# Kernel optimization log

Hardware: AMD Instinct MI355X
Metric: run time of the kernel (lower is better)

Reference implementation:

```python
import jax, jax.numpy as jnp
import numpy as np

N_NODES = 100000
N_EDGES = 3200000
N_FEAT = 500
N_HID = 256
N_CLASS = 40


def spmm(edge_row, edge_col, edge_val, x, num_nodes):
    # out[i] = sum_{e: row[e]==i} val[e] * x[col[e]]
    msgs = edge_val[:, None] * x[edge_col]          # [E, F] gather + scale
    return jax.ops.segment_sum(msgs, edge_row, num_segments=num_nodes)


def setup_inputs() -> dict:
    key = jax.random.key(0)
    k1, k2, k3, k4, k5, k6, k7, k8 = jax.random.split(key, 8)
    features = jax.random.normal(k1, (N_NODES, N_FEAT), dtype=jnp.float32)
    edge_row = jax.random.randint(k2, (N_EDGES,), 0, N_NODES, dtype=jnp.int32)
    edge_col = jax.random.randint(k3, (N_EDGES,), 0, N_NODES, dtype=jnp.int32)
    edge_val = jax.random.uniform(k4, (N_EDGES,), dtype=jnp.float32)
    # Xavier-uniform linear weights, zero biases (as in reset_parameters)
    lim1 = float(np.sqrt(6.0 / (N_FEAT + N_HID)))
    W1 = jax.random.uniform(k5, (N_FEAT, N_HID), minval=-lim1, maxval=lim1, dtype=jnp.float32)
    b1 = jnp.zeros((N_HID,), dtype=jnp.float32)
    lim2 = float(np.sqrt(6.0 / (N_HID + N_CLASS)))
    W2 = jax.random.uniform(k6, (N_HID, N_CLASS), minval=-lim2, maxval=lim2, dtype=jnp.float32)
    b2 = jnp.zeros((N_CLASS,), dtype=jnp.float32)
    return {
        "features": features,
        "edge_row": edge_row,
        "edge_col": edge_col,
        "edge_val": edge_val,
        "W1": W1, "b1": b1, "W2": W2, "b2": b2,
    }


def reference(features, edge_row, edge_col, edge_val, W1, b1, W2, b2):
    # Layer 1: linear -> spmm -> relu   (eval mode: dropout is identity)
    h = features @ W1 + b1                          # [N, nhid]
    h = spmm(edge_row, edge_col, edge_val, h, N_NODES)
    h = jax.nn.relu(h)
    # Layer 2: linear -> spmm
    o = h @ W2 + b2                                 # [N, nclass]
    o = spmm(edge_row, edge_col, edge_val, o, N_NODES)
    return jax.nn.log_softmax(o, axis=1)
```

## Files before the change

kernel.cpp:

```cpp
#include <hip/hip_runtime.h>
#include <hip/hip_bf16.h>
#include <math.h>

#define N_NODES 100000
#define N_FEAT 500
#define N_HID 256
#define N_CLASS 40

typedef float f32x4 __attribute__((ext_vector_type(4)));
typedef float f32x2 __attribute__((ext_vector_type(2)));
typedef int i32x4 __attribute__((ext_vector_type(4)));
typedef unsigned int u32x4 __attribute__((ext_vector_type(4)));
typedef short short8 __attribute__((ext_vector_type(8)));
typedef unsigned short u16x8 __attribute__((ext_vector_type(8)));

__device__ __forceinline__ float b2f(unsigned short u) {
  union { unsigned int i; float f; } c; c.i = ((unsigned int)u) << 16; return c.f;
}
__device__ __forceinline__ unsigned short f2bu(float x) {
  __hip_bfloat16 b = __float2bfloat16(x);
  union { __hip_bfloat16 b; unsigned short u; } c; c.b = b; return c.u;
}
__device__ __forceinline__ float decode_val(unsigned int p) {
  union { unsigned int i; float f; } c; c.i = (p & 0x7FFFu) << 17; return c.f;
}
__device__ __forceinline__ unsigned char f2fp8(float x) {
  return (unsigned char)(__builtin_amdgcn_cvt_pk_fp8_f32(x, x, 0, false) & 0xFF);
}
__device__ __forceinline__ void gload_lds16(const void* gptr, void* lptr) {
  __builtin_amdgcn_global_load_lds(
      (const __attribute__((address_space(1))) unsigned int*)gptr,
      (__attribute__((address_space(3))) unsigned int*)lptr, 16, 0, 0);
}

__global__ __launch_bounds__(256) void prep_kernel(
    const float* __restrict__ W1, unsigned short* __restrict__ Bsw,
    const int* __restrict__ er, const int* __restrict__ ec,
    const float* __restrict__ ev, int* __restrict__ cnt,
    unsigned int* __restrict__ cvps, int E) {
  if (blockIdx.x < 64) {
    int t = blockIdx.x * 256 + threadIdx.x;
    int col = t >> 6, ch = t & 63;
    int g = ch >> 3, c = ch & 7;
    int c_src = c ^ (col & 7);
    int k = g * 64 + c_src * 8;
    u16x8 o;
#pragma unroll
    for (int j = 0; j < 8; j++) {
      int kk = k + j;
      o[j] = (kk < N_FEAT) ? f2bu(W1[(size_t)kk * N_HID + col]) : (unsigned short)0;
    }
    *(u16x8*)(Bsw + (size_t)col * 512 + g * 64 + c * 8) = o;
  }
  int nv = E >> 2;
  int t = blockIdx.x * 256 + threadIdx.x;
  int nthr = gridDim.x * 256;
  const i32x4* er4 = (const i32x4*)er;
  const i32x4* ec4 = (const i32x4*)ec;
  const f32x4* ev4 = (const f32x4*)ev;
  for (int i = t; i < nv; i += nthr) {
    i32x4 r = __builtin_nontemporal_load(&er4[i]);
    i32x4 c = __builtin_nontemporal_load(&ec4[i]);
    f32x4 v = __builtin_nontemporal_load(&ev4[i]);
    atomicAdd(&cnt[r.x], 1);
    atomicAdd(&cnt[r.y], 1);
    atomicAdd(&cnt[r.z], 1);
    atomicAdd(&cnt[r.w], 1);
    u32x4 pk;
    pk.x = ((unsigned int)c.x << 15) | ((unsigned int)f2bu(v.x) >> 1);
    pk.y = ((unsigned int)c.y << 15) | ((unsigned int)f2bu(v.y) >> 1);
    pk.z = ((unsigned int)c.z << 15) | ((unsigned int)f2bu(v.z) >> 1);
    pk.w = ((unsigned int)c.w << 15) | ((unsigned int)f2bu(v.w) >> 1);
    __builtin_nontemporal_store(pk, (u32x4*)(cvps + 4 * (size_t)i));
  }
  int tail = nv << 2;
  if (blockIdx.x == 0 && threadIdx.x < E - tail) {
    int i = tail + threadIdx.x;
    atomicAdd(&cnt[er[i]], 1);
    cvps[i] = ((unsigned int)ec[i] << 15) | ((unsigned int)f2bu(ev[i]) >> 1);
  }
}

__global__ __launch_bounds__(1024) void scan1_kernel(
    int* __restrict__ cnt, int* __restrict__ bsum, int n) {
  __shared__ int wsum[16];
  int tid = threadIdx.x, lane = tid & 63, wid = tid >> 6;
  int i = blockIdx.x * 1024 + tid;
  int v = (i < n) ? cnt[i] : 0;
  int x = v;
#pragma unroll
  for (int off = 1; off < 64; off <<= 1) {
    int t = __shfl_up(x, off);
    if (lane >= off) x += t;
  }
  if (lane == 63) wsum[wid] = x;
  __syncthreads();
  if (tid < 16) {
    int ws = wsum[tid];
#pragma unroll
    for (int off = 1; off < 16; off <<= 1) {
      int t = __shfl_up(ws, off);
      if (tid >= off) ws += t;
    }
    wsum[tid] = ws;
  }
  __syncthreads();
  int excl = (wid ? wsum[wid - 1] : 0) + x - v;
  if (i < n) cnt[i] = excl;
  if (tid == 0) bsum[blockIdx.x] = wsum[15];
}

__global__ __launch_bounds__(64) void scan2_kernel(
    int* __restrict__ bsum, int* __restrict__ row_ptr, int nb, int n) {
  int lane = threadIdx.x;
  int carry = 0;
  for (int base = 0; base < nb; base += 64) {
    int i = base + lane;
    int v = (i < nb) ? bsum[i] : 0;
    int x = v;
#pragma unroll
    for (int off = 1; off < 64; off <<= 1) {
      int t = __shfl_up(x, off);
      if (lane >= off) x += t;
    }
    if (i < nb) bsum[i] = carry + x - v;
    carry += __shfl(x, 63);
  }
  if (lane == 0) row_ptr[n] = carry;
}

__global__ __launch_bounds__(256) void scan3_kernel(
    int* __restrict__ cnt, const int* __restrict__ bsum,
    int* __restrict__ row_ptr, int n) {
  int i = blockIdx.x * 256 + threadIdx.x;
  if (i >= n) return;
  int v = cnt[i] + bsum[i >> 10];
  cnt[i] = v;
  row_ptr[i] = v;
}

__global__ __launch_bounds__(256) void fused_sg(
    const int* __restrict__ er, const unsigned int* __restrict__ cvps,
    int* __restrict__ cursor, unsigned int* __restrict__ cvp, int E,
    const float* __restrict__ A, const unsigned short* __restrict__ Bsw,
    const float* __restrict__ b1, unsigned char* __restrict__ H, int M,
    int SB) {
  __shared__ __align__(16) char smem[36864];
  if ((int)blockIdx.x < SB) {
    int sb = blockIdx.x;
    int s = sb & 3;
    int g = sb >> 2;
    int ngrp = SB >> 2;
    int nv = E >> 2;
    const i32x4* er4 = (const i32x4*)er;
    const u32x4* cv4 = (const u32x4*)cvps;
    for (int i = g * 256 + threadIdx.x; i < nv; i += ngrp * 256) {
      i32x4 r = __builtin_nontemporal_load(&er4[i]);
      u32x4 p = __builtin_nontemporal_load(&cv4[i]);
      if (((r.x >> 9) & 3) == s) cvp[atomicAdd(&cursor[r.x], 1)] = p.x;
      if (((r.y >> 9) & 3) == s) cvp[atomicAdd(&cursor[r.y], 1)] = p.y;
      if (((r.z >> 9) & 3) == s) cvp[atomicAdd(&cursor[r.z], 1)] = p.z;
      if (((r.w >> 9) & 3) == s) cvp[atomicAdd(&cursor[r.w], 1)] = p.w;
    }
    int tail = nv << 2;
    if (sb == 0 && threadIdx.x < E - tail) {
      int i = tail + threadIdx.x;
      cvp[atomicAdd(&cursor[er[i]], 1)] = cvps[i];
    }
    return;
  }
  int gb = blockIdx.x - SB;
  char* sA = smem;
  char* sB = smem + 4096;
  int tid = threadIdx.x;
  int lane = tid & 63, w = tid >> 6;
  int wc = w;
  int bm = gb * 32;

  f32x4 acc[2][4];
#pragma unroll
  for (int m = 0; m < 2; m++)
#pragma unroll
    for (int n = 0; n < 4; n++) acc[m][n] = (f32x4)0.f;

  for (int s = 0; s < 8; s++) {
    int k0 = s * 64;
#pragma unroll
    for (int i = 0; i < 2; i++) {
      int f4 = i * 256 + tid;
      int row = f4 >> 4, cidx = f4 & 15;
      int grow = bm + row;
      int k = k0 + cidx * 4;
      float4 v = make_float4(0.f, 0.f, 0.f, 0.f);
      if (grow < M && k < N_FEAT) v = *(const float4*)(A + (size_t)grow * N_FEAT + k);
      ushort4 u;
      u.x = f2bu(v.x); u.y = f2bu(v.y); u.z = f2bu(v.z); u.w = f2bu(v.w);
      int chunk = cidx >> 1, sub = cidx & 1;
      int byte = row * 128 + (((chunk ^ (row & 7))) << 4) + (sub << 3);
      *(ushort4*)(sA + byte) = u;
    }
#pragma unroll
    for (int j = 0; j < 8; j++) {
      int base = j * 4096 + w * 1024;
      int L = base + lane * 16;
      int col = L >> 7, c = (L >> 4) & 7;
      const char* gp = (const char*)Bsw + (size_t)col * 1024 + s * 128 + c * 16;
      gload_lds16(gp, sB + base);
    }
    __syncthreads();
#pragma unroll
    for (int kk = 0; kk < 2; kk++) {
      int cw = kk * 4 + (lane >> 4);
      short8 af[2], bg[4];
#pragma unroll
      for (int m = 0; m < 2; m++) {
        int ar = m * 16 + (lane & 15);
        af[m] = *(const short8*)(sA + ar * 128 + ((cw ^ (ar & 7)) << 4));
      }
#pragma unroll
      for (int n = 0; n < 4; n++) {
        int bc = wc * 64 + n * 16 + (lane & 15);
        bg[n] = *(const short8*)(sB + bc * 128 + ((cw ^ (bc & 7)) << 4));
      }
#pragma unroll
      for (int m = 0; m < 2; m++)
#pragma unroll
        for (int n = 0; n < 4; n++)
          acc[m][n] = __builtin_amdgcn_mfma_f32_16x16x32_bf16(af[m], bg[n], acc[m][n], 0, 0, 0);
    }
    __syncthreads();
  }

  float bias[4];
#pragma unroll
  for (int n = 0; n < 4; n++) bias[n] = b1[wc * 64 + n * 16 + (lane & 15)];
#pragma unroll
  for (int m = 0; m < 2; m++) {
#pragma unroll
    for (int r = 0; r < 4; r++) {
      int row = bm + m * 16 + ((lane >> 4) << 2) + r;
      if (row < M) {
#pragma unroll
        for (int n = 0; n < 4; n++) {
          int col = wc * 64 + n * 16 + (lane & 15);
          H[(size_t)row * N_HID + col] = f2fp8(acc[m][n][r] + bias[n]);
        }
      }
    }
  }
}

__global__ __launch_bounds__(256) void spmm_fp8(
    const int* __restrict__ row_ptr, const unsigned int* __restrict__ cvp,
    const unsigned char* __restrict__ X, unsigned short* __restrict__ Y, int M) {
  int wave = (blockIdx.x * 256 + threadIdx.x) >> 6;
  int lane = threadIdx.x & 63;
  if (wave >= M) return;
  int start = row_ptr[wave], end = row_ptr[wave + 1];
  int qf = lane >> 4, fl = lane & 15;
  f32x4 a0 = (f32x4)0.f, a1 = (f32x4)0.f, a2 = (f32x4)0.f, a3 = (f32x4)0.f;
  const unsigned char* Xf = X + fl * 16;
#pragma unroll 2
  for (int e = start; e < end; e += 4) {
    int ei = e + qf;
    unsigned int p = (ei < end) ? cvp[ei] : 0u;
    float val = decode_val(p);
    size_t col = (size_t)(p >> 15);
    u32x4 d = *(const u32x4*)(Xf + col * N_HID);
    f32x2 f0 = __builtin_amdgcn_cvt_pk_f32_fp8(d.x, false);
    f32x2 f1 = __builtin_amdgcn_cvt_pk_f32_fp8(d.x, true);
    f32x2 f2 = __builtin_amdgcn_cvt_pk_f32_fp8(d.y, false);
    f32x2 f3 = __builtin_amdgcn_cvt_pk_f32_fp8(d.y, true);
    f32x2 f4 = __builtin_amdgcn_cvt_pk_f32_fp8(d.z, false);
    f32x2 f5 = __builtin_amdgcn_cvt_pk_f32_fp8(d.z, true);
    f32x2 f6 = __builtin_amdgcn_cvt_pk_f32_fp8(d.w, false);
    f32x2 f7 = __builtin_amdgcn_cvt_pk_f32_fp8(d.w, true);
    a0.x = fmaf(val, f0.x, a0.x); a0.y = fmaf(val, f0.y, a0.y);
    a0.z = fmaf(val, f1.x, a0.z); a0.w = fmaf(val, f1.y, a0.w);
    a1.x = fmaf(val, f2.x, a1.x); a1.y = fmaf(val, f2.y, a1.y);
    a1.z = fmaf(val, f3.x, a1.z); a1.w = fmaf(val, f3.y, a1.w);
    a2.x = fmaf(val, f4.x, a2.x); a2.y = fmaf(val, f4.y, a2.y);
    a2.z = fmaf(val, f5.x, a2.z); a2.w = fmaf(val, f5.y, a2.w);
    a3.x = fmaf(val, f6.x, a3.x); a3.y = fmaf(val, f6.y, a3.y);
    a3.z = fmaf(val, f7.x, a3.z); a3.w = fmaf(val, f7.y, a3.w);
  }
#define RED2(v) v += __shfl_xor(v, 16); v += __shfl_xor(v, 32);
  RED2(a0.x) RED2(a0.y) RED2(a0.z) RED2(a0.w)
  RED2(a1.x) RED2(a1.y) RED2(a1.z) RED2(a1.w)
  RED2(a2.x) RED2(a2.y) RED2(a2.z) RED2(a2.w)
  RED2(a3.x) RED2(a3.y) RED2(a3.z) RED2(a3.w)
#undef RED2
  if (qf == 0) {
    u16x8 o;
    o[0] = f2bu(fmaxf(a0.x, 0.f)); o[1] = f2bu(fmaxf(a0.y, 0.f));
    o[2] = f2bu(fmaxf(a0.z, 0.f)); o[3] = f2bu(fmaxf(a0.w, 0.f));
    o[4] = f2bu(fmaxf(a1.x, 0.f)); o[5] = f2bu(fmaxf(a1.y, 0.f));
    o[6] = f2bu(fmaxf(a1.z, 0.f)); o[7] = f2bu(fmaxf(a1.w, 0.f));
    *(u16x8*)(Y + (size_t)wave * N_HID + fl * 16) = o;
    o[0] = f2bu(fmaxf(a2.x, 0.f)); o[1] = f2bu(fmaxf(a2.y, 0.f));
    o[2] = f2bu(fmaxf(a2.z, 0.f)); o[3] = f2bu(fmaxf(a2.w, 0.f));
    o[4] = f2bu(fmaxf(a3.x, 0.f)); o[5] = f2bu(fmaxf(a3.y, 0.f));
    o[6] = f2bu(fmaxf(a3.z, 0.f)); o[7] = f2bu(fmaxf(a3.w, 0.f));
    *(u16x8*)(Y + (size_t)wave * N_HID + fl * 16 + 8) = o;
  }
}

__global__ __launch_bounds__(256) void gemm2_kernel(
    const unsigned short* __restrict__ H, const float* __restrict__ W2,
    const float* __restrict__ b2, unsigned short* __restrict__ O, int M) {
  __shared__ float Ws[N_HID * N_CLASS];
  __shared__ float sb2[N_CLASS];
  int tid = threadIdx.x;
  for (int i = tid; i < N_HID * N_CLASS; i += 256) Ws[i] = W2[i];
  if (tid < N_CLASS) sb2[tid] = b2[tid];
  __syncthreads();
  int r0 = (blockIdx.x * 256 + tid) * 2;
  if (r0 >= M) return;
  int r1 = r0 + 1;
  bool has1 = r1 < M;
  float acc0[N_CLASS], acc1[N_CLASS];
#pragma unroll
  for (int n = 0; n < N_CLASS; n++) { acc0[n] = sb2[n]; acc1[n] = sb2[n]; }
  const unsigned short* h0 = H + (size_t)r0 * N_HID;
  const unsigned short* h1 = H + (size_t)(has1 ? r1 : r0) * N_HID;
  for (int k0 = 0; k0 < N_HID; k0 += 8) {
    u16x8 va = *(const u16x8*)(h0 + k0);
    u16x8 vb = *(const u16x8*)(h1 + k0);
#pragma unroll
    for (int j = 0; j < 8; j++) {
      float a0 = b2f(va[j]), a1 = b2f(vb[j]);
      const float* wrow = &Ws[(k0 + j) * N_CLASS];
#pragma unroll
      for (int n = 0; n < N_CLASS; n++) {
        float wv = wrow[n];
        acc0[n] = fmaf(a0, wv, acc0[n]);
        acc1[n] = fmaf(a1, wv, acc1[n]);
      }
    }
  }
  unsigned short* o0 = O + (size_t)r0 * N_CLASS;
#pragma unroll
  for (int n = 0; n < N_CLASS; n += 4) {
    ushort4 p;
    p.x = f2bu(acc0[n]); p.y = f2bu(acc0[n + 1]);
    p.z = f2bu(acc0[n + 2]); p.w = f2bu(acc0[n + 3]);
    *(ushort4*)(o0 + n) = p;
  }
  if (has1) {
    unsigned short* o1 = O + (size_t)r1 * N_CLASS;
#pragma unroll
    for (int n = 0; n < N_CLASS; n += 4) {
      ushort4 p;
      p.x = f2bu(acc1[n]); p.y = f2bu(acc1[n + 1]);
      p.z = f2bu(acc1[n + 2]); p.w = f2bu(acc1[n + 3]);
      *(ushort4*)(o1 + n) = p;
    }
  }
}

__global__ __launch_bounds__(256) void spmm_csr_40_lsm(
    const int* __restrict__ row_ptr, const unsigned int* __restrict__ cvp,
    const unsigned short* __restrict__ X, float* __restrict__ Out, int M) {
  int wave = (blockIdx.x * 256 + threadIdx.x) >> 6;
  int lane = threadIdx.x & 63;
  if (wave >= M) return;
  int start = row_ptr[wave], end = row_ptr[wave + 1];
  bool act = lane < N_CLASS;
  int ln = act ? lane : 0;
  const unsigned short* Xc = X + ln;
  float acc = 0.f;
  int e = start;
  for (; e + 4 <= end; e += 4) {
    unsigned int p0 = cvp[e], p1 = cvp[e + 1], p2 = cvp[e + 2], p3 = cvp[e + 3];
    unsigned short x0 = Xc[(size_t)(p0 >> 15) * N_CLASS];
    unsigned short x1 = Xc[(size_t)(p1 >> 15) * N_CLASS];
    unsigned short x2 = Xc[(size_t)(p2 >> 15) * N_CLASS];
    unsigned short x3 = Xc[(size_t)(p3 >> 15) * N_CLASS];
    acc = fmaf(decode_val(p0), b2f(x0), acc);
    acc = fmaf(decode_val(p1), b2f(x1), acc);
    acc = fmaf(decode_val(p2), b2f(x2), acc);
    acc = fmaf(decode_val(p3), b2f(x3), acc);
  }
  for (; e < end; e++) {
    unsigned int p0 = cvp[e];
    acc = fmaf(decode_val(p0), b2f(Xc[(size_t)(p0 >> 15) * N_CLASS]), acc);
  }
  float mv = act ? acc : -INFINITY;
#pragma unroll
  for (int off = 32; off; off >>= 1) mv = fmaxf(mv, __shfl_xor(mv, off));
  float ex = act ? expf(acc - mv) : 0.f;
  float s = ex;
#pragma unroll
  for (int off = 32; off; off >>= 1) s += __shfl_xor(s, off);
  float lse = mv + logf(s);
  if (act) Out[(size_t)wave * N_CLASS + lane] = acc - lse;
}

extern "C" void kernel_launch(void* const* d_in, const int* in_sizes, int n_in,
                              void* d_out, int out_size, void* d_ws, size_t ws_size,
                              hipStream_t stream) {
  const float* feat = (const float*)d_in[0];
  const int* er     = (const int*)d_in[1];
  const int* ec     = (const int*)d_in[2];
  const float* ev   = (const float*)d_in[3];
  const float* W1   = (const float*)d_in[4];
  const float* b1   = (const float*)d_in[5];
  const float* W2   = (const float*)d_in[6];
  const float* b2   = (const float*)d_in[7];
  float* out = (float*)d_out;
  const int M = N_NODES;
  const int E = in_sizes[1];

  char* ws = (char*)d_ws;
  unsigned char* h      = (unsigned char*)(ws);
  unsigned short* hpost = (unsigned short*)(ws + 25600000);
  unsigned short* o     = (unsigned short*)(ws + 76800000);
  int* row_ptr          = (int*)(ws + 84800000);
  int* cursor           = (int*)(ws + 85200016);
  int* bsum             = (int*)(ws + 85600016);
  unsigned int* cvp     = (unsigned int*)(ws + 85600528);
  unsigned int* cvps    = (unsigned int*)(ws + 98400528);
  unsigned short* W1Tsw = (unsigned short*)(ws + 111200528);

  const int NB1 = (M + 1023) / 1024;
  const int SB = 2048;
  const int GB = (M + 31) / 32;

  (void)hipMemsetAsync(cursor, 0, (size_t)M * sizeof(int), stream);
  prep_kernel<<<1024, 256, 0, stream>>>(W1, W1Tsw, er, ec, ev, cursor, cvps, E);
  scan1_kernel<<<NB1, 1024, 0, stream>>>(cursor, bsum, M);
  scan2_kernel<<<1, 64, 0, stream>>>(bsum, row_ptr, NB1, M);
  scan3_kernel<<<(M + 255) / 256, 256, 0, stream>>>(cursor, bsum, row_ptr, M);
  fused_sg<<<SB + GB, 256, 0, stream>>>(er, cvps, cursor, cvp, E,
                                        feat, W1Tsw, b1, h, M, SB);
  spmm_fp8<<<(M + 3) / 4, 256, 0, stream>>>(row_ptr, cvp, h, hpost, M);
  gemm2_kernel<<<(M + 511) / 512, 256, 0, stream>>>(hpost, W2, b2, o, M);
  spmm_csr_40_lsm<<<(M + 3) / 4, 256, 0, stream>>>(row_ptr, cvp, o, out, M);
}
```

Baseline: 642.3 us.

## Interleave scatter and GEMM blocks in fused launch for concurrent execution

Remaps block indices so that, out of every five blocks, two run the CSR scatter work and three run the layer-1 GEMM, instead of all scatter blocks preceding all GEMM blocks. The aim is to overlap the atomic-heavy, memory-bound scatter with the MFMA-bound GEMM on the same CUs rather than running them in sequence. The GEMM block offset uses a hardcoded constant (3103) that must match the number of GEMM tiles, so the mapping is fragile if sizes or the scatter block count change.

```diff
diff --git a/kernel.cpp b/kernel.cpp
--- a/kernel.cpp
+++ b/kernel.cpp
@@ -146,36 +146,47 @@
     const float* __restrict__ b1, unsigned char* __restrict__ H, int M,
     int SB) {
   __shared__ __align__(16) char smem[36864];
-  if ((int)blockIdx.x < SB) {
-    int sb = blockIdx.x;
-    int s = sb & 3;
-    int g = sb >> 2;
+  int b = blockIdx.x;
+  int q = b / 5, r = b - q * 5;
+  bool is_scatter = false;
+  int sid = 0, gid = 0;
+  if (r < 2) {
+    int s = q * 2 + r;
+    if (s < SB) { is_scatter = true; sid = s; }
+    else gid = 3103 + (s - SB);
+  } else {
+    gid = q * 3 + (r - 2);
+  }
+
+  if (is_scatter) {
+    int s = sid & 3;
+    int g = sid >> 2;
     int ngrp = SB >> 2;
     int nv = E >> 2;
     const i32x4* er4 = (const i32x4*)er;
     const u32x4* cv4 = (const u32x4*)cvps;
     for (int i = g * 256 + threadIdx.x; i < nv; i += ngrp * 256) {
-      i32x4 r = __builtin_nontemporal_load(&er4[i]);
+      i32x4 rr = __builtin_nontemporal_load(&er4[i]);
       u32x4 p = __builtin_nontemporal_load(&cv4[i]);
-      if (((r.x >> 9) & 3) == s) cvp[atomicAdd(&cursor[r.x], 1)] = p.x;
-      if (((r.y >> 9) & 3) == s) cvp[atomicAdd(&cursor[r.y], 1)] = p.y;
-      if (((r.z >> 9) & 3) == s) cvp[atomicAdd(&cursor[r.z], 1)] = p.z;
-      if (((r.w >> 9) & 3) == s) cvp[atomicAdd(&cursor[r.w], 1)] = p.w;
+      if (((rr.x >> 9) & 3) == s) cvp[atomicAdd(&cursor[rr.x], 1)] = p.x;
+      if (((rr.y >> 9) & 3) == s) cvp[atomicAdd(&cursor[rr.y], 1)] = p.y;
+      if (((rr.z >> 9) & 3) == s) cvp[atomicAdd(&cursor[rr.z], 1)] = p.z;
+      if (((rr.w >> 9) & 3) == s) cvp[atomicAdd(&cursor[rr.w], 1)] = p.w;
     }
     int tail = nv << 2;
-    if (sb == 0 && threadIdx.x < E - tail) {
+    if (sid == 0 && threadIdx.x < E - tail) {
       int i = tail + threadIdx.x;
       cvp[atomicAdd(&cursor[er[i]], 1)] = cvps[i];
     }
     return;
   }
-  int gb = blockIdx.x - SB;
   char* sA = smem;
   char* sB = smem + 4096;
   int tid = threadIdx.x;
   int lane = tid & 63, w = tid >> 6;
   int wc = w;
-  int bm = gb * 32;
+  int bm = gid * 32;
+  if (bm >= M) return;
 
   f32x4 acc[2][4];
 #pragma unroll
@@ -237,13 +248,13 @@
 #pragma unroll
   for (int m = 0; m < 2; m++) {
 #pragma unroll
-    for (int r = 0; r < 4; r++) {
-      int row = bm + m * 16 + ((lane >> 4) << 2) + r;
+    for (int r2 = 0; r2 < 4; r2++) {
+      int row = bm + m * 16 + ((lane >> 4) << 2) + r2;
       if (row < M) {
 #pragma unroll
         for (int n = 0; n < 4; n++) {
           int col = wc * 64 + n * 16 + (lane & 15);
-          H[(size_t)row * N_HID + col] = f2fp8(acc[m][n][r] + bias[n]);
+          H[(size_t)row * N_HID + col] = f2fp8(acc[m][n][r2] + bias[n]);
         }
       }
     }
```

Result: no change. 647.5 us (+0.8%).
